# Kernel optimization log

Hardware: AMD Instinct MI355X
Metric: run time of the kernel (lower is better)

## Reference

```python
import jax, jax.numpy as jnp
import numpy as np

B, L, IN, HID, D3 = 32, 8192, 512, 512, 128

def setup_inputs() -> dict:
    key = jax.random.key(0)
    ks = jax.random.split(key, 7)
    s_in = 1.0 / np.sqrt(IN)
    s_h = 1.0 / np.sqrt(HID)
    return {
        'inputs': jax.random.normal(ks[0], (B, IN), jnp.float32),
        'context': jax.random.normal(ks[1], (B, L, HID), jnp.float32),
        'Wi': jax.random.uniform(ks[2], (D3, IN), jnp.float32, -s_in, s_in),
        'bi': jax.random.uniform(ks[3], (D3,), jnp.float32, -s_in, s_in),
        'Wh': jax.random.uniform(ks[4], (D3, HID), jnp.float32, -s_h, s_h),
        'bh': jax.random.uniform(ks[5], (D3,), jnp.float32, -s_h, s_h),
        'V': jax.random.uniform(ks[6], (D3,), jnp.float32, -1.0, 1.0),
    }

def reference(inputs, context, Wi, bi, Wh, bh, V):
    # inputs: (B, IN) -> (B, 1, D3); context: (B, L, HID) -> (B, L, D3)
    q = (inputs @ Wi.T + bi)[:, None, :]
    k = jnp.einsum('blh,dh->bld', context, Wh) + bh
    a = jnp.tanh(q + k)                              # (B, L, D3)
    att_row = jnp.einsum('bld,d->bl', a, V)[:, None, :]  # (B, 1, L)
    # NOTE: original applies softmax over dim=1 (the singleton dim) -> all ones.
    att = jax.nn.softmax(att_row, axis=1).squeeze(1)     # (B, L), faithful quirk
    return (att_row, att)
```

## Files before the change

### kernel.cpp

```cpp
#include <hip/hip_runtime.h>

typedef __attribute__((ext_vector_type(8))) short short8;
typedef __attribute__((ext_vector_type(8))) unsigned short ushort8;
typedef __attribute__((ext_vector_type(4))) float f32x4;

#define B_   32
#define L_   8192
#define IN_  512
#define HID_ 512
#define D3_  128

static __device__ __forceinline__ short f2bf(float f) {
    return __builtin_bit_cast(short, (__bf16)f);
}
static __device__ __forceinline__ unsigned short f2bfu(float f) {
    return __builtin_bit_cast(unsigned short, (__bf16)f);
}

__global__ void prep_whb2(const float* __restrict__ wh, unsigned short* __restrict__ whb2) {
    int u = blockIdx.x * 256 + threadIdx.x;
    int lane = u & 63;
    int nt   = (u >> 6) & 7;
    int ks   = u >> 9;
    int col  = nt * 16 + (lane & 15);
    int k0   = ks * 32 + (lane >> 4) * 8;
    const float* src = wh + col * HID_ + k0;
    float4 a = *(const float4*)(src);
    float4 b = *(const float4*)(src + 4);
    unsigned short* d = whb2 + (size_t)u * 8;
    d[0] = f2bfu(a.x); d[1] = f2bfu(a.y); d[2] = f2bfu(a.z); d[3] = f2bfu(a.w);
    d[4] = f2bfu(b.x); d[5] = f2bfu(b.y); d[6] = f2bfu(b.z); d[7] = f2bfu(b.w);
}

__global__ void prep_qpb(const float* __restrict__ inputs, const float* __restrict__ Wi,
                         const float* __restrict__ bi, const float* __restrict__ bh,
                         float* __restrict__ qpb) {
    int b = blockIdx.x;
    int d = threadIdx.x;
    float acc = bi[d] + bh[d];
    const float* xr = inputs + b * IN_;
    const float* wr = Wi + d * IN_;
    #pragma unroll 4
    for (int i = 0; i < IN_; i += 4) {
        float4 x = *(const float4*)(xr + i);
        float4 w = *(const float4*)(wr + i);
        acc += x.x * w.x + x.y * w.y + x.z * w.z + x.w * w.w;
    }
    qpb[b * D3_ + d] = acc;
}

__global__ __launch_bounds__(512) void attn_main(
    const float* __restrict__ ctx, const unsigned short* __restrict__ whb2,
    const float* __restrict__ qpb, const float* __restrict__ V,
    float* __restrict__ out)
{
    __shared__ unsigned short whs[D3_ * HID_];

    const int tid = threadIdx.x;

    #pragma unroll
    for (int p = 0; p < 16; ++p) {
        int m = p * 512 + tid;
        *(ushort8*)((char*)whs + (size_t)m * 16) = *(const ushort8*)(whb2 + (size_t)m * 8);
    }
    __syncthreads();

    const int lane = tid & 63;
    const int w    = tid >> 6;
    const int cb   = lane & 15;
    const int g    = lane >> 4;

    const char* bptr = (const char*)whs + lane * 16;

    const float* pL = ctx + ((size_t)blockIdx.x * 1024 + w * 16 + cb) * (size_t)HID_ + g * 8;

    const int b = blockIdx.x >> 3;

    float vv[8], qv[8];
    #pragma unroll
    for (int nt = 0; nt < 8; ++nt) {
        vv[nt] = V[nt * 16 + cb];
        qv[nt] = qpb[b * D3_ + nt * 16 + cb];
    }

#define DOSTEP(PA, PB, KK) { \
    short8 aA; \
    aA[0] = f2bf(PA.x); aA[1] = f2bf(PA.y); aA[2] = f2bf(PA.z); aA[3] = f2bf(PA.w); \
    aA[4] = f2bf(PB.x); aA[5] = f2bf(PB.y); aA[6] = f2bf(PB.z); aA[7] = f2bf(PB.w); \
    if ((KK) < 14) { \
        PA = *(const float4*)(pT + ((KK) + 2) * 32); \
        PB = *(const float4*)(pT + ((KK) + 2) * 32 + 4); \
    } else { \
        PA = *(const float4*)(pN + ((KK) - 14) * 32); \
        PB = *(const float4*)(pN + ((KK) - 14) * 32 + 4); \
    } \
    __builtin_amdgcn_sched_barrier(0); \
    _Pragma("unroll") \
    for (int nt = 0; nt < 8; ++nt) { \
        const short8 bb = *(const short8*)(bptr + (KK) * 8192 + nt * 1024); \
        acc[nt] = __builtin_amdgcn_mfma_f32_16x16x32_bf16(aA, bb, acc[nt], 0, 0, 0); \
    } \
    _Pragma("unroll") \
    for (int q8 = 0; q8 < 8; ++q8) { \
        __builtin_amdgcn_sched_group_barrier(0x100, 1, 0);  \
        __builtin_amdgcn_sched_group_barrier(0x008, 1, 0);  \
    } }

    float4 E0 = *(const float4*)(pL);        float4 E1 = *(const float4*)(pL + 4);
    float4 O0 = *(const float4*)(pL + 32);   float4 O1 = *(const float4*)(pL + 36);

    #pragma unroll 1
    for (int t = 0; t < 8; ++t) {
        const float* pT = pL + (size_t)t * (128 * HID_);
        const float* pN = (t < 7) ? (pT + 128 * HID_) : pL;

        f32x4 acc[8];
        #pragma unroll
        for (int nt = 0; nt < 8; ++nt) acc[nt] = (f32x4){0.f, 0.f, 0.f, 0.f};

        DOSTEP(E0, E1, 0)   DOSTEP(O0, O1, 1)
        DOSTEP(E0, E1, 2)   DOSTEP(O0, O1, 3)
        DOSTEP(E0, E1, 4)   DOSTEP(O0, O1, 5)
        DOSTEP(E0, E1, 6)   DOSTEP(O0, O1, 7)
        DOSTEP(E0, E1, 8)   DOSTEP(O0, O1, 9)
        DOSTEP(E0, E1, 10)  DOSTEP(O0, O1, 11)
        DOSTEP(E0, E1, 12)  DOSTEP(O0, O1, 13)
        DOSTEP(E0, E1, 14)  DOSTEP(O0, O1, 15)

        float s0 = 0.f, s1 = 0.f, s2 = 0.f, s3 = 0.f;
        #pragma unroll
        for (int nt = 0; nt < 8; ++nt) {
            const float q = qv[nt], vn = vv[nt];
            s0 += (1.f - 2.f / (__expf(2.f * (acc[nt][0] + q)) + 1.f)) * vn;
            s1 += (1.f - 2.f / (__expf(2.f * (acc[nt][1] + q)) + 1.f)) * vn;
            s2 += (1.f - 2.f / (__expf(2.f * (acc[nt][2] + q)) + 1.f)) * vn;
            s3 += (1.f - 2.f / (__expf(2.f * (acc[nt][3] + q)) + 1.f)) * vn;
        }
        #pragma unroll
        for (int m = 1; m < 16; m <<= 1) {
            s0 += __shfl_xor(s0, m, 64);
            s1 += __shfl_xor(s1, m, 64);
            s2 += __shfl_xor(s2, m, 64);
            s3 += __shfl_xor(s3, m, 64);
        }
        if (cb == 0) {
            const size_t row0 = (size_t)blockIdx.x * 1024 + (size_t)t * 128 + w * 16;
            const size_t off_ = row0 + (size_t)g * 4;
            *(float4*)(out + off_) = make_float4(s0, s1, s2, s3);
            *(float4*)(out + (size_t)B_ * L_ + off_) = make_float4(1.f, 1.f, 1.f, 1.f);
        }
    }
#undef DOSTEP
}

extern "C" void kernel_launch(void* const* d_in, const int* in_sizes, int n_in,
                              void* d_out, int out_size, void* d_ws, size_t ws_size,
                              hipStream_t stream) {
    const float* inputs  = (const float*)d_in[0];
    const float* context = (const float*)d_in[1];
    const float* Wi      = (const float*)d_in[2];
    const float* bi      = (const float*)d_in[3];
    const float* Wh      = (const float*)d_in[4];
    const float* bh      = (const float*)d_in[5];
    const float* V       = (const float*)d_in[6];
    float* out = (float*)d_out;

    unsigned short* whb2 = (unsigned short*)d_ws;
    float* qpb = (float*)((char*)d_ws + (size_t)D3_ * HID_ * 2);

    prep_whb2<<<32, 256, 0, stream>>>(Wh, whb2);
    prep_qpb<<<B_, D3_, 0, stream>>>(inputs, Wi, bi, bh, qpb);
    attn_main<<<256, 512, 0, stream>>>(context, whb2, qpb, V, out);
}
```

Measured before the change: 140.6 us.

## Deepen context prefetch to four k-steps and drop manual MFMA scheduling

Increases the register prefetch distance for context rows from two k-steps to four, with four rotating register pairs, so more global loads are in flight to hide HBM latency. It removes the sched_barrier and sched_group_barrier hints, leaving instruction interleaving to the compiler. It also reloads q and V from memory in the epilogue instead of keeping them in registers, which frees registers for the deeper prefetch at the cost of extra loads per tile.

After: 471.5 us. 235% more time.

```diff
diff --git a/kernel.cpp b/kernel.cpp
--- a/kernel.cpp
+++ b/kernel.cpp
@@ -76,38 +76,27 @@
 
     const int b = blockIdx.x >> 3;
 
-    float vv[8], qv[8];
-    #pragma unroll
-    for (int nt = 0; nt < 8; ++nt) {
-        vv[nt] = V[nt * 16 + cb];
-        qv[nt] = qpb[b * D3_ + nt * 16 + cb];
-    }
-
-#define DOSTEP(PA, PB, KK) { \
+#define STEPK(RA, RB, KK) { \
     short8 aA; \
-    aA[0] = f2bf(PA.x); aA[1] = f2bf(PA.y); aA[2] = f2bf(PA.z); aA[3] = f2bf(PA.w); \
-    aA[4] = f2bf(PB.x); aA[5] = f2bf(PB.y); aA[6] = f2bf(PB.z); aA[7] = f2bf(PB.w); \
-    if ((KK) < 14) { \
-        PA = *(const float4*)(pT + ((KK) + 2) * 32); \
-        PB = *(const float4*)(pT + ((KK) + 2) * 32 + 4); \
+    aA[0] = f2bf(RA.x); aA[1] = f2bf(RA.y); aA[2] = f2bf(RA.z); aA[3] = f2bf(RA.w); \
+    aA[4] = f2bf(RB.x); aA[5] = f2bf(RB.y); aA[6] = f2bf(RB.z); aA[7] = f2bf(RB.w); \
+    if ((KK) < 12) { \
+        RA = *(const float4*)(pT + ((KK) + 4) * 32); \
+        RB = *(const float4*)(pT + ((KK) + 4) * 32 + 4); \
     } else { \
-        PA = *(const float4*)(pN + ((KK) - 14) * 32); \
-        PB = *(const float4*)(pN + ((KK) - 14) * 32 + 4); \
+        RA = *(const float4*)(pN + ((KK) - 12) * 32); \
+        RB = *(const float4*)(pN + ((KK) - 12) * 32 + 4); \
     } \
-    __builtin_amdgcn_sched_barrier(0); \
     _Pragma("unroll") \
     for (int nt = 0; nt < 8; ++nt) { \
         const short8 bb = *(const short8*)(bptr + (KK) * 8192 + nt * 1024); \
         acc[nt] = __builtin_amdgcn_mfma_f32_16x16x32_bf16(aA, bb, acc[nt], 0, 0, 0); \
-    } \
-    _Pragma("unroll") \
-    for (int q8 = 0; q8 < 8; ++q8) { \
-        __builtin_amdgcn_sched_group_barrier(0x100, 1, 0);  \
-        __builtin_amdgcn_sched_group_barrier(0x008, 1, 0);  \
     } }
 
-    float4 E0 = *(const float4*)(pL);        float4 E1 = *(const float4*)(pL + 4);
-    float4 O0 = *(const float4*)(pL + 32);   float4 O1 = *(const float4*)(pL + 36);
+    float4 R0a = *(const float4*)(pL);         float4 R0b = *(const float4*)(pL + 4);
+    float4 R1a = *(const float4*)(pL + 32);    float4 R1b = *(const float4*)(pL + 36);
+    float4 R2a = *(const float4*)(pL + 64);    float4 R2b = *(const float4*)(pL + 68);
+    float4 R3a = *(const float4*)(pL + 96);    float4 R3b = *(const float4*)(pL + 100);
 
     #pragma unroll 1
     for (int t = 0; t < 8; ++t) {
@@ -118,19 +107,20 @@
         #pragma unroll
         for (int nt = 0; nt < 8; ++nt) acc[nt] = (f32x4){0.f, 0.f, 0.f, 0.f};
 
-        DOSTEP(E0, E1, 0)   DOSTEP(O0, O1, 1)
-        DOSTEP(E0, E1, 2)   DOSTEP(O0, O1, 3)
-        DOSTEP(E0, E1, 4)   DOSTEP(O0, O1, 5)
-        DOSTEP(E0, E1, 6)   DOSTEP(O0, O1, 7)
-        DOSTEP(E0, E1, 8)   DOSTEP(O0, O1, 9)
-        DOSTEP(E0, E1, 10)  DOSTEP(O0, O1, 11)
-        DOSTEP(E0, E1, 12)  DOSTEP(O0, O1, 13)
-        DOSTEP(E0, E1, 14)  DOSTEP(O0, O1, 15)
+        STEPK(R0a, R0b, 0)   STEPK(R1a, R1b, 1)
+        STEPK(R2a, R2b, 2)   STEPK(R3a, R3b, 3)
+        STEPK(R0a, R0b, 4)   STEPK(R1a, R1b, 5)
+        STEPK(R2a, R2b, 6)   STEPK(R3a, R3b, 7)
+        STEPK(R0a, R0b, 8)   STEPK(R1a, R1b, 9)
+        STEPK(R2a, R2b, 10)  STEPK(R3a, R3b, 11)
+        STEPK(R0a, R0b, 12)  STEPK(R1a, R1b, 13)
+        STEPK(R2a, R2b, 14)  STEPK(R3a, R3b, 15)
 
         float s0 = 0.f, s1 = 0.f, s2 = 0.f, s3 = 0.f;
         #pragma unroll
         for (int nt = 0; nt < 8; ++nt) {
-            const float q = qv[nt], vn = vv[nt];
+            const float q  = qpb[b * D3_ + nt * 16 + cb];
+            const float vn = V[nt * 16 + cb];
             s0 += (1.f - 2.f / (__expf(2.f * (acc[nt][0] + q)) + 1.f)) * vn;
             s1 += (1.f - 2.f / (__expf(2.f * (acc[nt][1] + q)) + 1.f)) * vn;
             s2 += (1.f - 2.f / (__expf(2.f * (acc[nt][2] + q)) + 1.f)) * vn;
@@ -150,7 +140,7 @@
             *(float4*)(out + (size_t)B_ * L_ + off_) = make_float4(1.f, 1.f, 1.f, 1.f);
         }
     }
-#undef DOSTEP
+#undef STEPK
 }
 
 extern "C" void kernel_launch(void* const* d_in, const int* in_sizes, int n_in,
```
